# Performance work log

Measured on AMD Instinct MI355X. Metric: run time of the kernel, lower is better.

## Reference

```python
import jax, jax.numpy as jnp
import numpy as np

VOCAB = 256
EMBED = 1024
HIDDEN = 1024
LAYERS = 2
RATIO = 0.25
R_GATE = int(4 * HIDDEN * RATIO)   # low-rank dim of the 4H gate projection
R_DEC = int(VOCAB * RATIO)         # low-rank dim of decoder
BATCH, SEQ = 64, 256


def setup_inputs() -> dict:
    key = jax.random.key(0)
    ks = jax.random.split(key, 16)
    stdv = 1.0 / np.sqrt(HIDDEN)
    u = lambda k, shape, s: jax.random.uniform(k, shape, jnp.float32, -s, s)
    tokens = jax.random.randint(ks[0], (BATCH, SEQ), 0, VOCAB)
    embed = jax.random.normal(ks[1], (VOCAB, EMBED), jnp.float32)
    # per-layer low-rank LSTM params, stacked over layers (embed==hidden)
    VT_ih = u(ks[2], (LAYERS, R_GATE, HIDDEN), stdv)
    bVT_ih = u(ks[3], (LAYERS, R_GATE), stdv)
    U_ih = u(ks[4], (LAYERS, 4 * HIDDEN, R_GATE), stdv)
    bU_ih = u(ks[5], (LAYERS, 4 * HIDDEN), stdv)
    VT_hh = u(ks[6], (LAYERS, R_GATE, HIDDEN), stdv)
    bVT_hh = u(ks[7], (LAYERS, R_GATE), stdv)
    U_hh = u(ks[8], (LAYERS, 4 * HIDDEN, R_GATE), stdv)
    bU_hh = u(ks[9], (LAYERS, 4 * HIDDEN), stdv)
    # decoder LowRankLinear (nn.Linear default-ish init scale)
    s1 = 1.0 / np.sqrt(HIDDEN)
    s2 = 1.0 / np.sqrt(R_DEC)
    dec_VT = u(ks[10], (R_DEC, HIDDEN), s1)
    dec_bVT = u(ks[11], (R_DEC,), s1)
    dec_U = u(ks[12], (VOCAB, R_DEC), s2)
    dec_bU = u(ks[13], (VOCAB,), s2)
    return dict(tokens=tokens, embed=embed, VT_ih=VT_ih, bVT_ih=bVT_ih,
                U_ih=U_ih, bU_ih=bU_ih, VT_hh=VT_hh, bVT_hh=bVT_hh,
                U_hh=U_hh, bU_hh=bU_hh, dec_VT=dec_VT, dec_bVT=dec_bVT,
                dec_U=dec_U, dec_bU=dec_bU)


def _lstm_layer(x_seq, p):
    # x_seq: [T, B, H]; p: tuple of this layer's params
    vt_ih, bvt_ih, u_ih, bu_ih, vt_hh, bvt_hh, u_hh, bu_hh = p
    B = x_seq.shape[1]
    H = u_ih.shape[0] // 4
    h0 = jnp.zeros((B, H), x_seq.dtype)
    c0 = jnp.zeros((B, H), x_seq.dtype)

    def step(carry, x):
        h, c = carry
        gates = ((x @ vt_ih.T + bvt_ih) @ u_ih.T + bu_ih
                 + (h @ vt_hh.T + bvt_hh) @ u_hh.T + bu_hh)   # [B, 4H]
        i, f, g, o = jnp.split(gates, 4, axis=-1)
        i = jax.nn.sigmoid(i)
        f = jax.nn.sigmoid(f)
        g = jnp.tanh(g)
        o = jax.nn.sigmoid(o)
        c_new = f * c + i * g
        h_new = o * jnp.tanh(c_new)
        return (h_new, c_new), h_new

    _, out = jax.lax.scan(step, (h0, c0), x_seq)
    return out  # [T, B, H]


def reference(tokens, embed, VT_ih, bVT_ih, U_ih, bU_ih, VT_hh, bVT_hh,
              U_hh, bU_hh, dec_VT, dec_bVT, dec_U, dec_bU):
    x = embed[tokens]                 # [B, T, E]
    x = jnp.transpose(x, (1, 0, 2))   # time-major [T, B, E]
    for l in range(LAYERS):
        p = (VT_ih[l], bVT_ih[l], U_ih[l], bU_ih[l],
             VT_hh[l], bVT_hh[l], U_hh[l], bU_hh[l])
        x = _lstm_layer(x, p)
    # low-rank decoder: [T, B, H] -> [T, B, V]
    logits = (x @ dec_VT.T + dec_bVT) @ dec_U.T + dec_bU
    return jnp.transpose(logits, (1, 2, 0))  # [B, V, T]
```

## Files before the change

### kernel.cpp

```cpp
#include <hip/hip_runtime.h>
#include <hip/hip_bf16.h>


#define B_SZ   64
#define T_SEQ  256
#define HID    1024
#define G4     4096

typedef __attribute__((ext_vector_type(8))) short bf16x8;
typedef __attribute__((ext_vector_type(4))) float f32x4;
typedef __attribute__((ext_vector_type(4))) short bf16x4;
typedef unsigned long long u64;

__device__ __forceinline__ f32x4 mfma16(bf16x8 a, bf16x8 b, f32x4 c) {
  return __builtin_amdgcn_mfma_f32_16x16x32_bf16(a, b, c, 0, 0, 0);
}
__device__ __forceinline__ float sigm(float x)  { return 1.f / (1.f + __expf(-x)); }
__device__ __forceinline__ float tanh_(float x) { return 2.f / (1.f + __expf(-2.f * x)) - 1.f; }
__device__ __forceinline__ f32x4 fzero() { f32x4 z; z[0]=0.f; z[1]=0.f; z[2]=0.f; z[3]=0.f; return z; }

__device__ __forceinline__ bf16x8 lda(const __hip_bfloat16* p) {
  const u64* q = (const u64*)p;
  union { u64 u[2]; bf16x8 v; } r;
  r.u[0] = __hip_atomic_load(q,     __ATOMIC_RELAXED, __HIP_MEMORY_SCOPE_AGENT);
  r.u[1] = __hip_atomic_load(q + 1, __ATOMIC_RELAXED, __HIP_MEMORY_SCOPE_AGENT);
  return r.v;
}

__device__ __forceinline__ float ld1(const void* p, size_t i, int mode) {
  return mode ? ((const float*)p)[i]
              : __bfloat162float(((const __hip_bfloat16*)p)[i]);
}
__device__ __forceinline__ bf16x8 ld8(const void* p, size_t i, int mode) {
  if (mode) {
    const float* f = (const float*)p + i;
    float4 a = *(const float4*)f;
    float4 b = *(const float4*)(f + 4);
    union { bf16x8 v; __hip_bfloat16 h[8]; } u;
    u.h[0] = __float2bfloat16(a.x); u.h[1] = __float2bfloat16(a.y);
    u.h[2] = __float2bfloat16(a.z); u.h[3] = __float2bfloat16(a.w);
    u.h[4] = __float2bfloat16(b.x); u.h[5] = __float2bfloat16(b.y);
    u.h[6] = __float2bfloat16(b.z); u.h[7] = __float2bfloat16(b.w);
    return u.v;
  }
  return *(const bf16x8*)((const __hip_bfloat16*)p + i);
}

__global__ void k_detect(const unsigned short* __restrict__ e, int* __restrict__ flags) {
  __shared__ int cnt;
  if (threadIdx.x == 0) cnt = 0;
  __syncthreads();
  int c = 0;
  for (int i = threadIdx.x; i < 2048; i += 256) {
    unsigned int bits = ((unsigned int)e[2 * i]) << 16;
    float f = __uint_as_float(bits);
    if (!isfinite(f) || fabsf(f) > 1e10f) ++c;
  }
  atomicAdd(&cnt, c);
  __syncthreads();
  if (threadIdx.x == 0) flags[0] = (cnt > 8) ? 1 : 0;
}

__global__ void k_cvt_b(const void* __restrict__ src, __hip_bfloat16* __restrict__ dst,
                        int n, const int* __restrict__ flags) {
  const int mode = flags[0];
  for (int i = blockIdx.x * blockDim.x + threadIdx.x; i < n; i += gridDim.x * blockDim.x)
    dst[i] = mode ? __float2bfloat16(((const float*)src)[i])
                  : ((const __hip_bfloat16*)src)[i];
}
__global__ void k_cvt_f(const void* __restrict__ src, float* __restrict__ dst,
                        int n, const int* __restrict__ flags) {
  const int mode = flags[0];
  for (int i = blockIdx.x * blockDim.x + threadIdx.x; i < n; i += gridDim.x * blockDim.x)
    dst[i] = mode ? ((const float*)src)[i]
                  : __bfloat162float(((const __hip_bfloat16*)src)[i]);
}

__global__ void k_init(unsigned* bar) {
  for (int i = threadIdx.x; i < 1024; i += 256) bar[i] = 0u;
}

__global__ void __launch_bounds__(256) k_combine(
    const void* __restrict__ U_ih, const void* __restrict__ U_hh,
    const void* __restrict__ VT_ih, const void* __restrict__ VT_hh,
    __hip_bfloat16* __restrict__ Wc, const int* __restrict__ flags)
{
  __shared__ __hip_bfloat16 sB[4 * 64 * 8];
  const int mode = flags[0];
  const int idx  = blockIdx.x;
  const int Mid  = idx >> 10;
  const int rem  = idx & 1023;
  const int gblk = rem >> 4, kblk = rem & 15;
  const int L = Mid >> 1, typ = Mid & 1;
  const void* U  = typ ? U_hh  : U_ih;
  const void* VT = typ ? VT_hh : VT_ih;
  const size_t Uoff  = (size_t)L * G4 * HID;
  const size_t VToff = (size_t)L * HID * HID;
  const int tid = threadIdx.x, lane = tid & 63, wv = tid >> 6;

  f32x4 acc[4];
  for (int i = 0; i < 4; ++i) acc[i] = fzero();

  const int r_local = tid >> 3;
  const int kk8     = (tid & 7) * 8;

  for (int r0 = 0; r0 < HID; r0 += 32) {
    union { bf16x8 v; __hip_bfloat16 h[8]; } u;
    u.v = ld8(VT, VToff + (size_t)(r0 + r_local) * HID + kblk * 64 + kk8, mode);
    __syncthreads();
    #pragma unroll
    for (int j = 0; j < 8; ++j) {
      int k_local = kk8 + j;
      int tile = k_local >> 4;
      int ln   = ((r_local >> 3) << 4) | (k_local & 15);
      sB[(tile * 64 + ln) * 8 + (r_local & 7)] = u.h[j];
    }
    __syncthreads();
    bf16x8 a = ld8(U, Uoff + (size_t)(gblk * 64 + wv * 16 + (lane & 15)) * HID
                          + r0 + (lane >> 4) * 8, mode);
    #pragma unroll
    for (int nt = 0; nt < 4; ++nt) {
      bf16x8 b = *(const bf16x8*)(sB + (nt * 64 + lane) * 8);
      acc[nt] = mfma16(a, b, acc[nt]);
    }
  }
  #pragma unroll
  for (int nt = 0; nt < 4; ++nt)
    #pragma unroll
    for (int r = 0; r < 4; ++r) {
      int g = gblk * 64 + wv * 16 + (lane >> 4) * 4 + r;
      int k = kblk * 64 + nt * 16 + (lane & 15);
      Wc[((size_t)Mid * G4 + g) * HID + k] = __float2bfloat16(acc[nt][r]);
    }
}

__global__ void __launch_bounds__(256) k_bias(
    const void* __restrict__ bVT_ih, const void* __restrict__ U_ih,
    const void* __restrict__ bU_ih,
    const void* __restrict__ bVT_hh, const void* __restrict__ U_hh,
    const void* __restrict__ bU_hh,
    float* __restrict__ bc, const int* __restrict__ flags)
{
  const int mode  = flags[0];
  const int g_all = blockIdx.x * 4 + (threadIdx.x >> 6);
  const int lane  = threadIdx.x & 63;
  const int L = g_all >> 12, g = g_all & 4095;
  const size_t ub = (size_t)(L * G4 + g) * HID + lane * 16;
  const size_t vb = (size_t)L * HID + lane * 16;
  float s = 0.f;
  #pragma unroll
  for (int c = 0; c < 16; ++c)
    s += ld1(bVT_ih, vb + c, mode) * ld1(U_ih, ub + c, mode)
       + ld1(bVT_hh, vb + c, mode) * ld1(U_hh, ub + c, mode);
  for (int off = 32; off; off >>= 1) s += __shfl_down(s, off);
  if (lane == 0)
    bc[g_all] = s + ld1(bU_ih, L * G4 + g, mode) + ld1(bU_hh, L * G4 + g, mode);
}

__global__ void __launch_bounds__(256, 1) k_lstm(
    const int* __restrict__ tokens, const __hip_bfloat16* __restrict__ embedC,
    const __hip_bfloat16* __restrict__ Wc, const float* __restrict__ bc,
    __hip_bfloat16* __restrict__ H1, __hip_bfloat16* __restrict__ H2,
    unsigned* bar, const int h1mask, const int cmode)
{
  extern __shared__ char smem[];
  __hip_bfloat16* Wl = (__hip_bfloat16*)smem;
  f32x4* Xex = (f32x4*)(smem + 131072);
  __hip_bfloat16* Hs = (__hip_bfloat16*)(smem + 139264);

  const int tid  = threadIdx.x;
  const int lane = tid & 63, wv = tid >> 6;
  const int w    = blockIdx.x;
  const int L    = w >> 7, jg = w & 127;
  const int mat  = wv >> 1, mhalf = wv & 1;
  const bool leaderWave = (jg == 0) && (wv == 0);

  for (int q = tid; q < 8192; q += 256) {
    int m_ = q >> 12, ks = (q >> 7) & 31, tl = (q >> 6) & 1, ln = q & 63;
    int n_local = tl * 16 + (ln & 15);
    int g = (n_local >> 3) * 1024 + jg * 8 + (n_local & 7);
    int k = ks * 32 + (ln >> 4) * 8;
    *(bf16x8*)(Wl + (size_t)q * 8) =
        *(const bf16x8*)(Wc + (((size_t)(L * 2 + m_) * G4 + g) << 10) + k);
  }
  const int nb = lane & 7;
  const float b_i = bc[L * G4 +        jg * 8 + nb];
  const float b_f = bc[L * G4 + 1024 + jg * 8 + nb];
  const float b_g = bc[L * G4 + 2048 + jg * 8 + nb];
  const float b_o = bc[L * G4 + 3072 + jg * 8 + nb];
  __syncthreads();

  float cst[2][4] = {{0.f,0.f,0.f,0.f},{0.f,0.f,0.f,0.f}};
  const int m0 = mhalf * 32 + (lane & 15);
  const int ko = (lane >> 4) * 8;
  const __hip_bfloat16* wbase = Wl + mat * 32768;
  unsigned* Xrel = bar + 256 + L * 128;

  for (int t = 0; t < T_SEQ; ++t) {
    if (leaderWave) {
      const u64* own = (const u64*)bar + (L ? 64 : 0);
      const u64* oth = (const u64*)bar + (L ? 0 : 64);
      const unsigned need = (unsigned)t;
      for (;;) {
        u64 a = __hip_atomic_load(&own[lane], __ATOMIC_RELAXED, __HIP_MEMORY_SCOPE_AGENT);
        bool ok = ((unsigned)a >= need) && ((unsigned)(a >> 32) >= need);
        if (L == 1) {
          u64 b = __hip_atomic_load(&oth[lane], __ATOMIC_RELAXED, __HIP_MEMORY_SCOPE_AGENT);
          ok = ok && ((unsigned)b >= need + 1) && ((unsigned)(b >> 32) >= need + 1);
        } else if (cmode == 0) {
          u64 b = __hip_atomic_load(&oth[lane], __ATOMIC_RELAXED, __HIP_MEMORY_SCOPE_AGENT);
          ok = ok && ((unsigned)b + 3u >= need) && ((unsigned)(b >> 32) + 3u >= need);
        }
        if (__all(ok)) break;
        __builtin_amdgcn_s_sleep(1);
      }
      if (lane < 8)
        __hip_atomic_store(&Xrel[lane * 16], (unsigned)(t + 1),
                           __ATOMIC_RELAXED, __HIP_MEMORY_SCOPE_AGENT);
    } else if (L == 1 || mat == 1) {
      if (lane == 0) {
        for (;;) {
          unsigned v = __hip_atomic_load(&Xrel[(w & 7) * 16],
                                         __ATOMIC_RELAXED, __HIP_MEMORY_SCOPE_AGENT);
          if (v >= (unsigned)(t + 1)) break;
          __builtin_amdgcn_s_sleep(2);
        }
      }
    }

    f32x4 acc00 = fzero(), acc01 = fzero(), acc10 = fzero(), acc11 = fzero();
    bool doGemm = true, cached = false;
    const __hip_bfloat16 *A0 = nullptr, *A1 = nullptr;
    if (mat == 0) {
      if (L == 0) {
        A0 = embedC + ((size_t)tokens[m0 * T_SEQ + t] << 10);
        A1 = embedC + ((size_t)tokens[(m0 + 16) * T_SEQ + t] << 10);
        cached = true;
      } else {
        A0 = H1 + ((((size_t)(t & h1mask)) * 64 + m0) << 10);
        A1 = A0 + ((size_t)16 << 10);
        cached = (cmode != 0);
      }
    } else {
      if (t == 0) doGemm = false;
      else {
        if (L == 0) {
          A0 = H1 + ((((size_t)((t - 1) & h1mask)) * 64 + m0) << 10);
          cached = (cmode != 0);
        } else {
          A0 = H2 + (((size_t)(t - 1) * 64 + m0) << 10);
          cached = true;
        }
        A1 = A0 + ((size_t)16 << 10);
      }
    }
    if (doGemm) {
      if (cached) {
        bf16x8 p0[32], p1[32];
        #pragma unroll
        for (int i = 0; i < 32; ++i) {
          p0[i] = *(const bf16x8*)(A0 + i * 32 + ko);
          p1[i] = *(const bf16x8*)(A1 + i * 32 + ko);
        }
        __builtin_amdgcn_sched_barrier(0);
        #pragma unroll
        for (int ks = 0; ks < 32; ++ks) {
          bf16x8 b0 = *(const bf16x8*)(wbase + (ks * 2 + 0) * 512 + lane * 8);
          bf16x8 b1 = *(const bf16x8*)(wbase + (ks * 2 + 1) * 512 + lane * 8);
          acc00 = mfma16(p0[ks], b0, acc00);
          acc01 = mfma16(p0[ks], b1, acc01);
          acc10 = mfma16(p1[ks], b0, acc10);
          acc11 = mfma16(p1[ks], b1, acc11);
        }
      } else {
        #pragma unroll 4
        for (int ks = 0; ks < 32; ++ks) {
          bf16x8 a0 = lda(A0 + ks * 32 + ko);
          bf16x8 a1 = lda(A1 + ks * 32 + ko);
          bf16x8 b0 = *(const bf16x8*)(wbase + (ks * 2 + 0) * 512 + lane * 8);
          bf16x8 b1 = *(const bf16x8*)(wbase + (ks * 2 + 1) * 512 + lane * 8);
          acc00 = mfma16(a0, b0, acc00);
          acc01 = mfma16(a0, b1, acc01);
          acc10 = mfma16(a1, b0, acc10);
          acc11 = mfma16(a1, b1, acc11);
        }
      }
    }
    if (mat == 0) {
      Xex[(mhalf * 4 + 0) * 64 + lane] = acc00;
      Xex[(mhalf * 4 + 1) * 64 + lane] = acc01;
      Xex[(mhalf * 4 + 2) * 64 + lane] = acc10;
      Xex[(mhalf * 4 + 3) * 64 + lane] = acc11;
    }
    __syncthreads();
    if (mat == 1) {
      #pragma unroll
      for (int mt = 0; mt < 2; ++mt) {
        f32x4 aT0 = mt ? acc10 : acc00;
        f32x4 aT1 = mt ? acc11 : acc01;
        f32x4 gx0 = Xex[(mhalf * 4 + mt * 2 + 0) * 64 + lane];
        f32x4 gx1 = Xex[(mhalf * 4 + mt * 2 + 1) * 64 + lane];
        #pragma unroll
        for (int r = 0; r < 4; ++r) {
          float v0 = aT0[r] + gx0[r];
          float v1 = aT1[r] + gx1[r];
          float p0 = __shfl_xor(v0, 8);
          float p1 = __shfl_xor(v1, 8);
          if ((lane & 15) < 8) {
            float iv = sigm(v0 + b_i);
            float fv = sigm(p0 + b_f);
            float gv = tanh_(v1 + b_g);
            float ov = sigm(p1 + b_o);
            float c  = fv * cst[mt][r] + iv * gv;
            cst[mt][r] = c;
            float h  = ov * tanh_(c);
            int m = mhalf * 32 + mt * 16 + (lane >> 4) * 4 + r;
            Hs[m * 8 + (lane & 15)] = __float2bfloat16(h);
          }
        }
      }
    }
    __syncthreads();
    if (tid < 128) {
      char* HoutB = (L == 0) ? (char*)(H1 + (((size_t)(t & h1mask)) << 16))
                             : (char*)(H2 + (((size_t)t) << 16));
      u64 v = ((const u64*)Hs)[tid];
      u64* dst = (u64*)(HoutB + ((size_t)(tid >> 1) << 11) + (jg << 4) + ((tid & 1) << 3));
      __hip_atomic_store(dst, v, __ATOMIC_RELAXED, __HIP_MEMORY_SCOPE_AGENT);
    }
    __syncthreads();
    if (wv == 0 && lane == 0)
      __hip_atomic_store(&bar[w], (unsigned)(t + 1),
                         __ATOMIC_RELAXED, __HIP_MEMORY_SCOPE_AGENT);
  }
}

__global__ void __launch_bounds__(256) k_dec1(
    const __hip_bfloat16* __restrict__ H2, const __hip_bfloat16* __restrict__ dec_VTC,
    const float* __restrict__ dbv, __hip_bfloat16* __restrict__ R)
{
  const int t = blockIdx.x;
  const int lane = threadIdx.x & 63, wv = threadIdx.x >> 6;
  const __hip_bfloat16* A = H2 + ((size_t)t << 16) + ((size_t)(wv * 16 + (lane & 15)) << 10);
  const int ko = (lane >> 4) * 8;
  f32x4 acc[4];
  for (int i = 0; i < 4; ++i) acc[i] = fzero();
  for (int ks = 0; ks < 32; ++ks) {
    bf16x8 a = *(const bf16x8*)(A + ks * 32 + ko);
    #pragma unroll
    for (int nt = 0; nt < 4; ++nt) {
      bf16x8 b = *(const bf16x8*)(dec_VTC + ((size_t)(nt * 16 + (lane & 15)) << 10) + ks * 32 + ko);
      acc[nt] = mfma16(a, b, acc[nt]);
    }
  }
  #pragma unroll
  for (int nt = 0; nt < 4; ++nt) {
    int n = nt * 16 + (lane & 15);
    float bias = dbv[n];
    #pragma unroll
    for (int r = 0; r < 4; ++r) {
      int b_row = wv * 16 + (lane >> 4) * 4 + r;
      R[((size_t)t << 12) + (size_t)b_row * 64 + n] = __float2bfloat16(acc[nt][r] + bias);
    }
  }
}

__global__ void __launch_bounds__(256) k_dec2(
    const __hip_bfloat16* __restrict__ R, const __hip_bfloat16* __restrict__ dec_UC,
    const float* __restrict__ dbu, void* __restrict__ out,
    const int* __restrict__ flags)
{
  const int mode = flags[0];
  const int bblk = blockIdx.x >> 4, tblk = blockIdx.x & 15;
  const int lane = threadIdx.x & 63, wv = threadIdx.x >> 6;
  const int ko  = (lane >> 4) * 8;
  const int t_l = lane & 15;
  for (int bi = 0; bi < 4; ++bi) {
    const int b = bblk * 16 + wv * 4 + bi;
    f32x4 acc[16];
    for (int i = 0; i < 16; ++i) acc[i] = fzero();
    #pragma unroll
    for (int ks = 0; ks < 2; ++ks) {
      bf16x8 a = *(const bf16x8*)(R + (((size_t)(tblk * 16 + t_l) * 64 + b) << 6)
                                    + ks * 32 + ko);
      #pragma unroll
      for (int nt = 0; nt < 16; ++nt) {
        bf16x8 bb = *(const bf16x8*)(dec_UC + ((size_t)(nt * 16 + t_l) << 6) + ks * 32 + ko);
        acc[nt] = mfma16(a, bb, acc[nt]);
      }
    }
    #pragma unroll
    for (int nt = 0; nt < 16; ++nt) {
      int v = nt * 16 + t_l;
      float bias = dbu[v];
      size_t off = (size_t)b * 65536 + (size_t)v * 256 + tblk * 16 + (lane >> 4) * 4;
      if (mode) {
        float4 st;
        st.x = acc[nt][0] + bias; st.y = acc[nt][1] + bias;
        st.z = acc[nt][2] + bias; st.w = acc[nt][3] + bias;
        *(float4*)((float*)out + off) = st;
      } else {
        union { bf16x4 v4; __hip_bfloat16 h[4]; } u;
        #pragma unroll
        for (int r = 0; r < 4; ++r) u.h[r] = __float2bfloat16(acc[nt][r] + bias);
        *(bf16x4*)((__hip_bfloat16*)out + off) = u.v4;
      }
    }
  }
}

extern "C" void kernel_launch(void* const* d_in, const int* in_sizes, int n_in,
                              void* d_out, int out_size, void* d_ws, size_t ws_size,
                              hipStream_t stream)
{
  const int* tokens  = (const int*)d_in[0];
  const void* embed  = d_in[1];
  const void* VT_ih  = d_in[2];
  const void* bVT_ih = d_in[3];
  const void* U_ih   = d_in[4];
  const void* bU_ih  = d_in[5];
  const void* VT_hh  = d_in[6];
  const void* bVT_hh = d_in[7];
  const void* U_hh   = d_in[8];
  const void* bU_hh  = d_in[9];
  const void* dec_VT = d_in[10];
  const void* dec_bVT= d_in[11];
  const void* dec_U  = d_in[12];
  const void* dec_bU = d_in[13];

  char* ws = (char*)d_ws;
  const size_t M = 1024 * 1024;
  __hip_bfloat16* Wc      = (__hip_bfloat16*)ws;
  __hip_bfloat16* H2      = (__hip_bfloat16*)(ws + 32 * M);
  char* aux = ws + 64 * M;
  int*            flags   = (int*)aux;
  float*          bc      = (float*)(aux + 4096);
  float*          dbv     = (float*)(aux + 36864);
  float*          dbu     = (float*)(aux + 37120);
  __hip_bfloat16* embedC  = (__hip_bfloat16*)(aux + 65536);
  __hip_bfloat16* dec_VTC = (__hip_bfloat16*)(aux + 589824);
  __hip_bfloat16* dec_UC  = (__hip_bfloat16*)(aux + 720896);
  __hip_bfloat16* H1ring  = (__hip_bfloat16*)(aux + 1048576);
  unsigned*       bar     = (unsigned*)(aux + 1572864);
  __hip_bfloat16* R       = (__hip_bfloat16*)(aux + 2097152);
  __hip_bfloat16* H1big   = (__hip_bfloat16*)(ws + 68 * M);

  (void)in_sizes; (void)n_in; (void)out_size;

  const int big = (ws_size >= (size_t)100 * M);
  __hip_bfloat16* H1 = big ? H1big : H1ring;
  const int h1mask = big ? 255 : 3;
  const int cmode  = big ? 1 : 0;

  hipFuncSetAttribute((const void*)k_lstm,
                      hipFuncAttributeMaxDynamicSharedMemorySize, 140288);

  k_detect<<<1, 256, 0, stream>>>((const unsigned short*)embed, flags);
  k_cvt_b<<<256, 256, 0, stream>>>(embed,  embedC,  256 * 1024, flags);
  k_cvt_b<<<64,  256, 0, stream>>>(dec_VT, dec_VTC, 64 * 1024,  flags);
  k_cvt_b<<<16,  256, 0, stream>>>(dec_U,  dec_UC,  256 * 64,   flags);
  k_cvt_f<<<1,   64,  0, stream>>>(dec_bVT, dbv, 64,  flags);
  k_cvt_f<<<1,   256, 0, stream>>>(dec_bU,  dbu, 256, flags);
  k_combine<<<4096, 256, 0, stream>>>(U_ih, U_hh, VT_ih, VT_hh, Wc, flags);
  k_bias   <<<2048, 256, 0, stream>>>(bVT_ih, U_ih, bU_ih, bVT_hh, U_hh, bU_hh, bc, flags);
  k_init   <<<1, 256, 0, stream>>>(bar);
  k_lstm   <<<256, 256, 140288, stream>>>(tokens, embedC, Wc, bc, H1, H2, bar,
                                          h1mask, cmode);
  k_dec1   <<<256, 256, 0, stream>>>(H2, dec_VTC, dbv, R);
  k_dec2   <<<64, 256, 0, stream>>>(R, dec_UC, dbu, d_out, flags);
}
```

Measured before the change: 3.288 ms.

## Replace per-block flag polling with striped atomic counters in cmode barrier

In the non-zero cmode path, each block now signals step completion by atomically incrementing one of four striped counters per layer, instead of storing a per-block flag. Waiters poll just four (or eight) counters against thresholds of 32*t, replacing the leader-wave scan of all 64 flags and the later Xrel relay. This is meant to cut the latency and cache traffic of the cross-block step barrier in the persistent LSTM kernel. It adds atomic contention on a few cache lines and relies on exact counter arithmetic and on the bar region being zeroed.

```diff
diff --git a/kernel.cpp b/kernel.cpp
--- a/kernel.cpp
+++ b/kernel.cpp
@@ -195,9 +195,35 @@
   const int ko = (lane >> 4) * 8;
   const __hip_bfloat16* wbase = Wl + mat * 32768;
   unsigned* Xrel = bar + 256 + L * 128;
+  const unsigned* cnt0 = bar + 512;
+  const unsigned* cnt1 = bar + 512 + 64;
 
   for (int t = 0; t < T_SEQ; ++t) {
-    if (leaderWave) {
+    if (cmode != 0) {
+      const unsigned* pa = nullptr; unsigned ta = 0;
+      const unsigned* pb = nullptr; unsigned tb = 0;
+      if (L == 0) {
+        if (mat == 1 && t > 0) {
+          pa = cnt0; ta = 32u * (unsigned)t;
+          if (t > 4) { pb = cnt1; tb = 32u * (unsigned)(t - 4); }
+        }
+      } else {
+        if (mat == 0) { pa = cnt0; ta = 32u * (unsigned)(t + 1); }
+        else if (t > 0) { pa = cnt1; ta = 32u * (unsigned)t; }
+      }
+      if (pa) {
+        const unsigned* p = nullptr; unsigned thr = 0;
+        if (lane < 4) { p = pa + lane * 16; thr = ta; }
+        else if (lane < 8 && pb) { p = pb + (lane - 4) * 16; thr = tb; }
+        for (;;) {
+          bool ok = true;
+          if (p) ok = (__hip_atomic_load(p, __ATOMIC_RELAXED,
+                                         __HIP_MEMORY_SCOPE_AGENT) >= thr);
+          if (__all(ok)) break;
+          __builtin_amdgcn_s_sleep(1);
+        }
+      }
+    } else if (leaderWave) {
       const u64* own = (const u64*)bar + (L ? 64 : 0);
       const u64* oth = (const u64*)bar + (L ? 0 : 64);
       const unsigned need = (unsigned)t;
@@ -207,7 +233,7 @@
         if (L == 1) {
           u64 b = __hip_atomic_load(&oth[lane], __ATOMIC_RELAXED, __HIP_MEMORY_SCOPE_AGENT);
           ok = ok && ((unsigned)b >= need + 1) && ((unsigned)(b >> 32) >= need + 1);
-        } else if (cmode == 0) {
+        } else {
           u64 b = __hip_atomic_load(&oth[lane], __ATOMIC_RELAXED, __HIP_MEMORY_SCOPE_AGENT);
           ok = ok && ((unsigned)b + 3u >= need) && ((unsigned)(b >> 32) + 3u >= need);
         }
@@ -329,9 +355,14 @@
       __hip_atomic_store(dst, v, __ATOMIC_RELAXED, __HIP_MEMORY_SCOPE_AGENT);
     }
     __syncthreads();
-    if (wv == 0 && lane == 0)
-      __hip_atomic_store(&bar[w], (unsigned)(t + 1),
-                         __ATOMIC_RELAXED, __HIP_MEMORY_SCOPE_AGENT);
+    if (tid == 0) {
+      if (cmode != 0)
+        __hip_atomic_fetch_add((unsigned*)(bar + 512 + L * 64 + (jg & 3) * 16), 1u,
+                               __ATOMIC_RELAXED, __HIP_MEMORY_SCOPE_AGENT);
+      else
+        __hip_atomic_store(&bar[w], (unsigned)(t + 1),
+                           __ATOMIC_RELAXED, __HIP_MEMORY_SCOPE_AGENT);
+    }
   }
 }
 
```

Result: slower. 4.001 ms (+21.7%).
